# Kernel optimization log

Measured on AMD Instinct MI355X. Metric: run time of the kernel, lower is better.

The kernel has to match this reference:

```python
import jax, jax.numpy as jnp
import numpy as np

DIM = 512
BATCH = 65536


def setup_inputs() -> dict:
    key = jax.random.key(0)
    k1, k2 = jax.random.split(key)
    pq = jax.random.normal(k1, (BATCH, 2 * DIM), dtype=jnp.float32)
    A = jax.random.normal(k2, (DIM, DIM), dtype=jnp.float32)
    return {"pq": pq, "A": A}


def reference(pq, A):
    # up_or_low == 'up': pterm_i = (A + A^T) @ q_i, qterm = 0
    # npq = [p + pterm, q]
    S = A + A.T  # symmetric (dim, dim)
    p = pq[:, :DIM]
    q = pq[:, DIM:]
    # torch.mv(S, q_i) for every row i  ==  q @ S.T  (single batched matvec/GEMM)
    pterm = jnp.einsum("bd,ed->be", q, S)
    return jnp.concatenate([p + pterm, q], axis=-1)
```

## Files before the change

### kernel.cpp

```cpp
#include <hip/hip_runtime.h>

#define DIM 512
#define BATCH 65536
#define BM 32
#define THREADS 512

typedef float f32x4 __attribute__((ext_vector_type(4)));
typedef float f32x16 __attribute__((ext_vector_type(16)));
typedef __bf16 bf16x8 __attribute__((ext_vector_type(8)));

__device__ __forceinline__ unsigned f2bf(float f) {
    unsigned u = __float_as_uint(f);
    return (u + 0x7FFFu + ((u >> 16) & 1u)) >> 16;
}

__global__ void prep_Sfrag(const float* __restrict__ A, unsigned short* __restrict__ Sf) {
    int idx = blockIdx.x * 256 + threadIdx.x;
    int lane = idx & 63;
    int np   = (idx >> 6) & 15;
    int k0   = idx >> 10;
    int n     = np * 32 + (lane & 31);
    int kbase = k0 * 16 + (lane >> 5) * 8;
    unsigned short tmp[8];
    #pragma unroll
    for (int j = 0; j < 8; ++j) {
        int k = kbase + j;
        tmp[j] = (unsigned short)f2bf(A[n * DIM + k] + A[k * DIM + n]);
    }
    *(uint4*)(Sf + (size_t)idx * 8) = *(const uint4*)tmp;
}

__global__ __launch_bounds__(THREADS, 8)
void gemm_kernel(const float* __restrict__ pq,
                 const unsigned short* __restrict__ Sf,
                 float* __restrict__ out) {
    __shared__ unsigned short qs[BM * DIM];
    const int rb  = blockIdx.x * BM;
    const int tid = threadIdx.x;
    const int wid  = tid >> 6;
    const int lane = tid & 63;
    const int row  = lane & 31;
    const int khalf = lane >> 5;

    #pragma unroll
    for (int i = 0; i < 8; ++i) {
        int flat = (tid + i * THREADS) * 4;
        int r = flat >> 9, c = flat & 511;
        size_t g = (size_t)(rb + r) * 1024 + 512 + c;
        f32x4 v = __builtin_nontemporal_load((const f32x4*)(pq + g));
        __builtin_nontemporal_store(v, (f32x4*)(out + g));
        unsigned lo = f2bf(v.x) | (f2bf(v.y) << 16);
        unsigned hi = f2bf(v.z) | (f2bf(v.w) << 16);
        int bo = (c * 2) ^ ((r & 15) << 4);
        *(uint2*)((char*)qs + r * 1024 + bo) = make_uint2(lo, hi);
    }
    __syncthreads();

    const unsigned short* Sfp = Sf + ((size_t)(wid * 2) * 64 + lane) * 8;
    f32x16 acc0 = {}, acc1 = {};
    #pragma unroll
    for (int k0 = 0; k0 < 32; ++k0) {
        int bo = (k0 * 32 + khalf * 16) ^ ((row & 15) << 4);
        bf16x8 a  = *(const bf16x8*)((const char*)qs + row * 1024 + bo);
        bf16x8 b0 = *(const bf16x8*)(Sfp + (size_t)k0 * 8192);
        bf16x8 b1 = *(const bf16x8*)(Sfp + (size_t)k0 * 8192 + 512);
        acc0 = __builtin_amdgcn_mfma_f32_32x32x16_bf16(a, b0, acc0, 0, 0, 0);
        acc1 = __builtin_amdgcn_mfma_f32_32x32x16_bf16(a, b1, acc1, 0, 0, 0);
    }

    float* sc = (float*)qs;
    __syncthreads();
    #pragma unroll
    for (int pass = 0; pass < 2; ++pass) {
        const f32x16& ac = pass ? acc1 : acc0;
        #pragma unroll
        for (int reg = 0; reg < 16; ++reg) {
            int r = (reg & 3) + 8 * (reg >> 2) + 4 * khalf;
            sc[r * 256 + wid * 32 + row] = ac[reg];
        }
        __syncthreads();
        #pragma unroll
        for (int j = 0; j < 4; ++j) {
            int c  = tid + j * 512;
            int r  = c >> 6, cc = c & 63;
            int gcol = (cc >> 3) * 64 + (cc & 7) * 4 + pass * 32;
            size_t g = (size_t)(rb + r) * 1024 + gcol;
            f32x4 v  = *(const f32x4*)(sc + r * 256 + cc * 4);
            f32x4 pv = __builtin_nontemporal_load((const f32x4*)(pq + g));
            __builtin_nontemporal_store(pv + v, (f32x4*)(out + g));
        }
        __syncthreads();
    }
}

extern "C" void kernel_launch(void* const* d_in, const int* in_sizes, int n_in,
                              void* d_out, int out_size, void* d_ws, size_t ws_size,
                              hipStream_t stream) {
    const float* pq = (const float*)d_in[0];
    const float* A  = (const float*)d_in[1];
    float* out = (float*)d_out;
    unsigned short* Sf = (unsigned short*)d_ws;

    prep_Sfrag<<<128, 256, 0, stream>>>(A, Sf);
    gemm_kernel<<<BATCH / BM, THREADS, 0, stream>>>(pq, Sf, out);
}
```

Before: 142.8 us.

## Make GEMM blocks persistent over four row tiles with double-buffered q loading

Each block now handles four 32-row tiles in sequence. The q half of pq is loaded in two K-halves into a double-buffered shared-memory area, so global loads for the next phase are in flight while MFMAs run on the current one. S fragments are register-prefetched one k-step ahead, the epilogue gets its own scratch buffer, and launch bounds drop to 4 blocks per SM. This aims to hide memory latency in a bandwidth-bound kernel, at the cost of fewer blocks for latency hiding and more registers.

```diff
diff --git a/kernel.cpp b/kernel.cpp
--- a/kernel.cpp
+++ b/kernel.cpp
@@ -4,6 +4,8 @@
 #define BATCH 65536
 #define BM 32
 #define THREADS 512
+#define TILES 4
+#define NBLK (BATCH / (BM * TILES))
 
 typedef float f32x4 __attribute__((ext_vector_type(4)));
 typedef float f32x16 __attribute__((ext_vector_type(16)));
@@ -30,66 +32,110 @@
     *(uint4*)(Sf + (size_t)idx * 8) = *(const uint4*)tmp;
 }
 
-__global__ __launch_bounds__(THREADS, 8)
+__global__ __launch_bounds__(THREADS, 4)
 void gemm_kernel(const float* __restrict__ pq,
                  const unsigned short* __restrict__ Sf,
                  float* __restrict__ out) {
-    __shared__ unsigned short qs[BM * DIM];
-    const int rb  = blockIdx.x * BM;
-    const int tid = threadIdx.x;
+    __shared__ __align__(16) unsigned short qh[2][BM * 256];
+    __shared__ float sc[BM * 256];
+    const int tid  = threadIdx.x;
     const int wid  = tid >> 6;
     const int lane = tid & 63;
     const int row  = lane & 31;
     const int khalf = lane >> 5;
+    const int rb = blockIdx.x * (BM * TILES);
+    const unsigned short* Sfp = Sf + ((size_t)(wid * 2) * 64 + lane) * 8;
+    const int col0 = wid * 64 + row;
+    (void)col0;
 
-    #pragma unroll
-    for (int i = 0; i < 8; ++i) {
-        int flat = (tid + i * THREADS) * 4;
-        int r = flat >> 9, c = flat & 511;
-        size_t g = (size_t)(rb + r) * 1024 + 512 + c;
-        f32x4 v = __builtin_nontemporal_load((const f32x4*)(pq + g));
-        __builtin_nontemporal_store(v, (f32x4*)(out + g));
-        unsigned lo = f2bf(v.x) | (f2bf(v.y) << 16);
-        unsigned hi = f2bf(v.z) | (f2bf(v.w) << 16);
-        int bo = (c * 2) ^ ((r & 15) << 4);
-        *(uint2*)((char*)qs + r * 1024 + bo) = make_uint2(lo, hi);
-    }
+    f32x4 stg[4];
+
+    auto issue_loads = [&](int ph) {
+        int tile = ph >> 1, half = ph & 1;
+        #pragma unroll
+        for (int i = 0; i < 2; ++i) {
+            int slot = i * THREADS + tid;
+            int r = slot >> 5, c8 = slot & 31;
+            size_t g = (size_t)(rb + tile * BM + r) * 1024 + 512 + half * 256 + c8 * 8;
+            stg[2*i]   = __builtin_nontemporal_load((const f32x4*)(pq + g));
+            stg[2*i+1] = __builtin_nontemporal_load((const f32x4*)(pq + g + 4));
+        }
+    };
+    auto write_back = [&](int ph) {
+        int tile = ph >> 1, half = ph & 1;
+        unsigned short* dst = qh[ph & 1];
+        #pragma unroll
+        for (int i = 0; i < 2; ++i) {
+            int slot = i * THREADS + tid;
+            int r = slot >> 5, c8 = slot & 31;
+            size_t g = (size_t)(rb + tile * BM + r) * 1024 + 512 + half * 256 + c8 * 8;
+            __builtin_nontemporal_store(stg[2*i],   (f32x4*)(out + g));
+            __builtin_nontemporal_store(stg[2*i+1], (f32x4*)(out + g + 4));
+            unsigned u0 = f2bf(stg[2*i].x)   | (f2bf(stg[2*i].y)   << 16);
+            unsigned u1 = f2bf(stg[2*i].z)   | (f2bf(stg[2*i].w)   << 16);
+            unsigned u2 = f2bf(stg[2*i+1].x) | (f2bf(stg[2*i+1].y) << 16);
+            unsigned u3 = f2bf(stg[2*i+1].z) | (f2bf(stg[2*i+1].w) << 16);
+            int b = r * 512 + ((c8 * 16) ^ ((r & 7) << 4));
+            *(uint4*)((char*)dst + b) = make_uint4(u0, u1, u2, u3);
+        }
+    };
+    auto khalf_loop = [&](int ph, f32x16& acc0, f32x16& acc1) {
+        int half = ph & 1;
+        const unsigned short* buf = qh[ph & 1];
+        const unsigned short* sp = Sfp + (size_t)(half * 16) * 8192;
+        bf16x8 b0_c = *(const bf16x8*)(sp);
+        bf16x8 b1_c = *(const bf16x8*)(sp + 512);
+        #pragma unroll
+        for (int k = 0; k < 16; ++k) {
+            bf16x8 b0_n, b1_n;
+            if (k < 15) {
+                b0_n = *(const bf16x8*)(sp + (size_t)(k + 1) * 8192);
+                b1_n = *(const bf16x8*)(sp + (size_t)(k + 1) * 8192 + 512);
+            }
+            int b = row * 512 + ((k * 32 + khalf * 16) ^ ((row & 7) << 4));
+            bf16x8 a = *(const bf16x8*)((const char*)buf + b);
+            acc0 = __builtin_amdgcn_mfma_f32_32x32x16_bf16(a, b0_c, acc0, 0, 0, 0);
+            acc1 = __builtin_amdgcn_mfma_f32_32x32x16_bf16(a, b1_c, acc1, 0, 0, 0);
+            if (k < 15) { b0_c = b0_n; b1_c = b1_n; }
+        }
+    };
+    auto epilogue = [&](int tile, const f32x16& acc0, const f32x16& acc1) {
+        int tb = rb + tile * BM;
+        #pragma unroll
+        for (int pass = 0; pass < 2; ++pass) {
+            const f32x16& ac = pass ? acc1 : acc0;
+            #pragma unroll
+            for (int reg = 0; reg < 16; ++reg) {
+                int r = (reg & 3) + 8 * (reg >> 2) + 4 * khalf;
+                sc[r * 256 + wid * 32 + row] = ac[reg];
+            }
+            __syncthreads();
+            #pragma unroll
+            for (int j = 0; j < 4; ++j) {
+                int c = tid + j * 512;
+                int r = c >> 6, cc = c & 63;
+                int gcol = (cc >> 3) * 64 + (cc & 7) * 4 + pass * 32;
+                size_t g = (size_t)(tb + r) * 1024 + gcol;
+                f32x4 v  = *(const f32x4*)(sc + r * 256 + cc * 4);
+                f32x4 pv = __builtin_nontemporal_load((const f32x4*)(pq + g));
+                __builtin_nontemporal_store(pv + v, (f32x4*)(out + g));
+            }
+            __syncthreads();
+        }
+    };
+
+    f32x16 acc0, acc1;
+    issue_loads(0);
+    write_back(0);
     __syncthreads();
 
-    const unsigned short* Sfp = Sf + ((size_t)(wid * 2) * 64 + lane) * 8;
-    f32x16 acc0 = {}, acc1 = {};
-    #pragma unroll
-    for (int k0 = 0; k0 < 32; ++k0) {
-        int bo = (k0 * 32 + khalf * 16) ^ ((row & 15) << 4);
-        bf16x8 a  = *(const bf16x8*)((const char*)qs + row * 1024 + bo);
-        bf16x8 b0 = *(const bf16x8*)(Sfp + (size_t)k0 * 8192);
-        bf16x8 b1 = *(const bf16x8*)(Sfp + (size_t)k0 * 8192 + 512);
-        acc0 = __builtin_amdgcn_mfma_f32_32x32x16_bf16(a, b0, acc0, 0, 0, 0);
-        acc1 = __builtin_amdgcn_mfma_f32_32x32x16_bf16(a, b1, acc1, 0, 0, 0);
-    }
-
-    float* sc = (float*)qs;
-    __syncthreads();
-    #pragma unroll
-    for (int pass = 0; pass < 2; ++pass) {
-        const f32x16& ac = pass ? acc1 : acc0;
-        #pragma unroll
-        for (int reg = 0; reg < 16; ++reg) {
-            int r = (reg & 3) + 8 * (reg >> 2) + 4 * khalf;
-            sc[r * 256 + wid * 32 + row] = ac[reg];
-        }
+    for (int ph = 0; ph < 2 * TILES; ++ph) {
+        if ((ph & 1) == 0) { acc0 = f32x16{}; acc1 = f32x16{}; }
+        if (ph + 1 < 2 * TILES) issue_loads(ph + 1);
+        khalf_loop(ph, acc0, acc1);
+        if (ph + 1 < 2 * TILES) write_back(ph + 1);
         __syncthreads();
-        #pragma unroll
-        for (int j = 0; j < 4; ++j) {
-            int c  = tid + j * 512;
-            int r  = c >> 6, cc = c & 63;
-            int gcol = (cc >> 3) * 64 + (cc & 7) * 4 + pass * 32;
-            size_t g = (size_t)(rb + r) * 1024 + gcol;
-            f32x4 v  = *(const f32x4*)(sc + r * 256 + cc * 4);
-            f32x4 pv = __builtin_nontemporal_load((const f32x4*)(pq + g));
-            __builtin_nontemporal_store(pv + v, (f32x4*)(out + g));
-        }
-        __syncthreads();
+        if (ph & 1) epilogue(ph >> 1, acc0, acc1);
     }
 }
 
@@ -102,5 +148,5 @@
     unsigned short* Sf = (unsigned short*)d_ws;
 
     prep_Sfrag<<<128, 256, 0, stream>>>(A, Sf);
-    gemm_kernel<<<BATCH / BM, THREADS, 0, stream>>>(pq, Sf, out);
+    gemm_kernel<<<NBLK, THREADS, 0, stream>>>(pq, Sf, out);
 }
```

Measured after the change: 131.7 us. 7.8% less time.
